# Optimization experiments

Measured on AMD Instinct MI355X. Metric: run time of the kernel, lower is better.

The kernel has to match this reference:

```python
import jax, jax.numpy as jnp
import numpy as np

B, T, D, H = 4096, 512, 5, 64
G = 4 * H  # i,f,g,o gates stacked (PyTorch order)
FC1, FC2 = 32, 1


def _uniform(key, shape, scale):
    return jax.random.uniform(key, shape, jnp.float32, -scale, scale)


def setup_inputs() -> dict:
    key = jax.random.key(0)
    ks = jax.random.split(key, 14)
    s = 1.0 / np.sqrt(H)  # torch LSTM/Linear init scale
    return {
        "x": jax.random.normal(ks[0], (B, T, D), jnp.float32),
        "W_ih0": _uniform(ks[1], (G, D), s),
        "W_hh0": _uniform(ks[2], (G, H), s),
        "b_ih0": _uniform(ks[3], (G,), s),
        "b_hh0": _uniform(ks[4], (G,), s),
        "W_ih1": _uniform(ks[5], (G, H), s),
        "W_hh1": _uniform(ks[6], (G, H), s),
        "b_ih1": _uniform(ks[7], (G,), s),
        "b_hh1": _uniform(ks[8], (G,), s),
        "W1": _uniform(ks[9], (FC1, H), s),
        "b1": _uniform(ks[10], (FC1,), s),
        "W2": _uniform(ks[11], (FC2, FC1), 1.0 / np.sqrt(FC1)),
        "b2": _uniform(ks[12], (FC2,), 1.0 / np.sqrt(FC1)),
    }


def lstm_layer(x, W_ih, W_hh, b_ih, b_hh):
    # x: [B,T,Din] -> (h_seq [B,T,H], h_T [B,H])
    b = x.shape[0]
    h = W_hh.shape[1]
    # precompute input contribution for all timesteps
    pre = jnp.einsum('btd,gd->btg', x, W_ih) + b_ih + b_hh  # [B,T,4H]

    def step(carry, xt):
        hs, cs = carry
        gates = xt + hs @ W_hh.T  # [B,4H]
        i, f, g, o = jnp.split(gates, 4, axis=-1)
        i = jax.nn.sigmoid(i)
        f = jax.nn.sigmoid(f)
        g = jnp.tanh(g)
        o = jax.nn.sigmoid(o)
        cs = f * cs + i * g
        hs = o * jnp.tanh(cs)
        return (hs, cs), hs

    h0 = jnp.zeros((b, h), x.dtype)
    (hT, cT), h_seq = jax.lax.scan(step, (h0, h0), jnp.swapaxes(pre, 0, 1))
    return jnp.swapaxes(h_seq, 0, 1), hT


def reference(x, W_ih0, W_hh0, b_ih0, b_hh0, W_ih1, W_hh1, b_ih1, b_hh1, W1, b1, W2, b2):
    # eval mode: dropout layers are identity
    h1_seq, _ = lstm_layer(x, W_ih0, W_hh0, b_ih0, b_hh0)
    _, h2_T = lstm_layer(h1_seq, W_ih1, W_hh1, b_ih1, b_hh1)  # h_n[-1]
    z = jax.nn.relu(h2_T @ W1.T + b1)  # [B,32]
    out = z @ W2.T + b2  # [B,1]
    return out.squeeze(-1)  # [B]
```

## Files before the change

### kernel.cpp

```cpp
#include <hip/hip_runtime.h>
#include <cstddef>

#define T_STEPS  512
#define D_IN     5
#define NB       16
#define NTHREADS 1024
#define LOG2E    1.4426950408889634f

typedef __attribute__((ext_vector_type(8))) short f16x8;
typedef __attribute__((ext_vector_type(4))) float f32x4;

#define MFMA_INIT(D, A, B, C) \
    asm("v_mfma_f32_16x16x32_f16 %0, %1, %2, %3" : "=&v"(D) : "a"(A), "v"(B), "v"(C))
#define MFMA_ACC(D, A, B) \
    asm("v_mfma_f32_16x16x32_f16 %0, %1, %2, %0" : "+v"(D) : "a"(A), "v"(B))

__device__ __forceinline__ short f2h(float f) {
    return (short)__builtin_bit_cast(unsigned short, (_Float16)f);
}

__device__ __forceinline__ float lstm_cell(const f32x4 acc, float& c) {
    const float tg = __builtin_amdgcn_exp2f(acc[2]);
    const float ui = __builtin_amdgcn_exp2f(-acc[0]);
    const float uf = __builtin_amdgcn_exp2f(-acc[1]);
    const float ig = (tg - 1.0f) * __builtin_amdgcn_rcpf((1.0f + ui) * (1.0f + tg));
    const float fz = __builtin_amdgcn_rcpf(1.0f + uf);
    c = fmaf(fz, c, ig);
    const float ca = fminf(c * (2.0f * LOG2E), 126.0f);
    const float tc = __builtin_amdgcn_exp2f(ca);
    const float uo = __builtin_amdgcn_exp2f(-acc[3]);
    return (tc - 1.0f) * __builtin_amdgcn_rcpf((1.0f + uo) * (1.0f + tc));
}

__device__ __forceinline__ int hswz(int n, int col) {
    return (((col >> 3) ^ (n & 7)) << 3) | (col & 7);
}

__global__ __launch_bounds__(NTHREADS, 4)
void lstm_stack_mfma7(const float* __restrict__ x,
                      const float* __restrict__ W_ih0,
                      const float* __restrict__ W_hh0,
                      const float* __restrict__ b_ih0,
                      const float* __restrict__ b_hh0,
                      const float* __restrict__ W_ih1,
                      const float* __restrict__ W_hh1,
                      const float* __restrict__ b_ih1,
                      const float* __restrict__ b_hh1,
                      const float* __restrict__ W1,
                      const float* __restrict__ b1,
                      const float* __restrict__ W2,
                      const float* __restrict__ b2,
                      float* __restrict__ out)
{
    __shared__ alignas(16) unsigned short h_hi[2][NB][128];
    __shared__ alignas(16) unsigned short x_pack[2][NB][40];
    __shared__ alignas(16) float h2f[NB][68];
    __shared__ alignas(16) float zb[NB][36];

    const int tid  = threadIdx.x;
    const int b0   = blockIdx.x * NB;
    const int w    = tid >> 6;
    const int lane = tid & 63;
    const int n16  = lane & 15;
    const int quad = lane >> 4;

    f16x8 aX;
    f16x8 a0[2];
    f16x8 a1[4];
    f32x4 bc0, bc1;
    float c0 = 0.f, c1 = 0.f;

    {
        const int u_a = w * 4 + (n16 >> 2);
        const int g_a = n16 & 3;
        const int r0  = g_a * 64 + u_a;
        const float sc = (g_a == 2) ? 2.0f * LOG2E : LOG2E;
        #pragma unroll
        for (int j = 0; j < 8; ++j) {
            const int k = quad * 8 + j;
            aX[j] = f2h(k < D_IN ? sc * W_ih0[r0 * D_IN + k] : 0.0f);
        }
        #pragma unroll
        for (int kt = 0; kt < 2; ++kt) {
            #pragma unroll
            for (int j = 0; j < 8; ++j)
                a0[kt][j] = f2h(sc * W_hh0[r0 * 64 + kt * 32 + quad * 8 + j]);
        }
        #pragma unroll
        for (int kt = 0; kt < 4; ++kt) {
            const int kg = kt * 32 + quad * 8;
            #pragma unroll
            for (int j = 0; j < 8; ++j)
                a1[kt][j] = f2h(sc * ((kg < 64) ? W_ih1[r0 * 64 + kg + j]
                                                : W_hh1[r0 * 64 + (kg - 64) + j]));
        }
        const int u_b = w * 4 + quad;
        #pragma unroll
        for (int r = 0; r < 4; ++r) {
            const float scr = (r == 2) ? 2.0f * LOG2E : LOG2E;
            bc0[r] = scr * (b_ih0[r * 64 + u_b] + b_hh0[r * 64 + u_b]);
            bc1[r] = scr * (b_ih1[r * 64 + u_b] + b_hh1[r * 64 + u_b]);
        }
    }

    for (int i = tid; i < 2 * NB * 128; i += NTHREADS) (&h_hi[0][0][0])[i] = 0;
    for (int i = tid; i < 2 * NB * 40; i += NTHREADS) (&x_pack[0][0][0])[i] = 0;
    __syncthreads();
    const int xb = tid / D_IN, xd = tid % D_IN;
    const bool xrole = (tid < NB * D_IN);
    if (xrole) {
        const float xv = x[((size_t)(b0 + xb) * T_STEPS) * D_IN + xd];
        x_pack[0][xb][xd] = (unsigned short)f2h(xv);
    }
    __syncthreads();

    const int u_c = w * 4 + quad;

    #pragma unroll 1
    for (int s = 0; s <= T_STEPS; ++s) {
        const int rb = s & 1, wbuf = rb ^ 1;

        float xv = 0.f;
        if (xrole && (s + 1) < T_STEPS)
            xv = x[((size_t)(b0 + xb) * T_STEPS + (s + 1)) * D_IN + xd];

        const f16x8 bxp = *reinterpret_cast<const f16x8*>(&x_pack[rb][n16][quad * 8]);
        f16x8 bhh[4];
        #pragma unroll
        for (int kt = 0; kt < 4; ++kt)
            bhh[kt] = *reinterpret_cast<const f16x8*>(
                &h_hi[rb][n16][((kt * 4 + quad) ^ (n16 & 7)) * 8]);

        f32x4 acc0, acc1;
        MFMA_INIT(acc0, aX, bxp, bc0);
        MFMA_ACC(acc0, a0[0], bhh[0]);
        MFMA_ACC(acc0, a0[1], bhh[1]);
        MFMA_INIT(acc1, a1[0], bhh[0], bc1);
        MFMA_ACC(acc1, a1[1], bhh[1]);
        MFMA_ACC(acc1, a1[2], bhh[2]);
        MFMA_ACC(acc1, a1[3], bhh[3]);

        asm("s_nop 7" : "+v"(acc0));
        if (s < T_STEPS) {
            const float h = lstm_cell(acc0, c0);
            h_hi[wbuf][n16][hswz(n16, u_c)] = (unsigned short)f2h(h);
        }

        asm("s_nop 7" : "+v"(acc1));
        if (s > 0) {
            const float h = lstm_cell(acc1, c1);
            h_hi[wbuf][n16][hswz(n16, 64 + u_c)] = (unsigned short)f2h(h);
            if (s == T_STEPS) h2f[n16][u_c] = h;
        }
        if (xrole && (s + 1) < T_STEPS)
            x_pack[wbuf][xb][xd] = (unsigned short)f2h(xv);
        __syncthreads();
    }

    if (tid < 512) {
        const int bb = tid >> 5;
        const int k  = tid & 31;
        float a = b1[k];
        #pragma unroll 16
        for (int j = 0; j < 64; ++j)
            a = fmaf(W1[k * 64 + j], h2f[bb][j], a);
        zb[bb][k] = fmaxf(a, 0.0f);
    }
    __syncthreads();
    if (tid < NB) {
        float a = b2[0];
        #pragma unroll
        for (int k = 0; k < 32; ++k) a = fmaf(W2[k], zb[tid][k], a);
        out[b0 + tid] = a;
    }
}

extern "C" void kernel_launch(void* const* d_in, const int* in_sizes, int n_in,
                              void* d_out, int out_size, void* d_ws, size_t ws_size,
                              hipStream_t stream) {
    (void)in_sizes; (void)n_in; (void)d_ws; (void)ws_size;
    const float* xp     = (const float*)d_in[0];
    const float* W_ih0  = (const float*)d_in[1];
    const float* W_hh0  = (const float*)d_in[2];
    const float* b_ih0  = (const float*)d_in[3];
    const float* b_hh0  = (const float*)d_in[4];
    const float* W_ih1  = (const float*)d_in[5];
    const float* W_hh1  = (const float*)d_in[6];
    const float* b_ih1  = (const float*)d_in[7];
    const float* b_hh1  = (const float*)d_in[8];
    const float* W1     = (const float*)d_in[9];
    const float* b1     = (const float*)d_in[10];
    const float* W2     = (const float*)d_in[11];
    const float* b2     = (const float*)d_in[12];
    float* outp = (float*)d_out;

    const int nblocks = out_size / NB;
    hipLaunchKernelGGL(lstm_stack_mfma7, dim3(nblocks), dim3(NTHREADS), 0, stream,
                       xp, W_ih0, W_hh0, b_ih0, b_hh0,
                       W_ih1, W_hh1, b_ih1, b_hh1,
                       W1, b1, W2, b2, outp);
}
```

Before: 533.4 us.

## Skew layer pipeline so off-critical-path MFMAs precompute next step's partial gates

```diff
diff --git a/kernel.cpp b/kernel.cpp
--- a/kernel.cpp
+++ b/kernel.cpp
@@ -23,21 +23,22 @@
     const float tg = __builtin_amdgcn_exp2f(acc[2]);
     const float ui = __builtin_amdgcn_exp2f(-acc[0]);
     const float uf = __builtin_amdgcn_exp2f(-acc[1]);
-    const float ig = (tg - 1.0f) * __builtin_amdgcn_rcpf((1.0f + ui) * (1.0f + tg));
-    const float fz = __builtin_amdgcn_rcpf(1.0f + uf);
-    c = fmaf(fz, c, ig);
+    const float A  = 1.0f + uf;
+    const float Bd = (1.0f + ui) * (1.0f + tg);
+    const float r  = __builtin_amdgcn_rcpf(A * Bd);
+    c = fmaf(c, Bd, (tg - 1.0f) * A) * r;
     const float ca = fminf(c * (2.0f * LOG2E), 126.0f);
     const float tc = __builtin_amdgcn_exp2f(ca);
     const float uo = __builtin_amdgcn_exp2f(-acc[3]);
     return (tc - 1.0f) * __builtin_amdgcn_rcpf((1.0f + uo) * (1.0f + tc));
 }
 
-__device__ __forceinline__ int hswz(int n, int col) {
-    return (((col >> 3) ^ (n & 7)) << 3) | (col & 7);
+__device__ __forceinline__ int hswz8(int n, int u) {
+    return (((u >> 3) ^ (n & 7)) << 3) | (u & 7);
 }
 
 __global__ __launch_bounds__(NTHREADS, 4)
-void lstm_stack_mfma7(const float* __restrict__ x,
+void lstm_stack_mfma8(const float* __restrict__ x,
                       const float* __restrict__ W_ih0,
                       const float* __restrict__ W_hh0,
                       const float* __restrict__ b_ih0,
@@ -52,7 +53,8 @@
                       const float* __restrict__ b2,
                       float* __restrict__ out)
 {
-    __shared__ alignas(16) unsigned short h_hi[2][NB][128];
+    __shared__ alignas(16) unsigned short h1b[2][NB][64];
+    __shared__ alignas(16) unsigned short h2b[2][NB][64];
     __shared__ alignas(16) unsigned short x_pack[2][NB][40];
     __shared__ alignas(16) float h2f[NB][68];
     __shared__ alignas(16) float zb[NB][36];
@@ -66,7 +68,8 @@
 
     f16x8 aX;
     f16x8 a0[2];
-    f16x8 a1[4];
+    f16x8 a1h1[2];
+    f16x8 a1h2[2];
     f32x4 bc0, bc1;
     float c0 = 0.f, c1 = 0.f;
 
@@ -83,16 +86,12 @@
         #pragma unroll
         for (int kt = 0; kt < 2; ++kt) {
             #pragma unroll
-            for (int j = 0; j < 8; ++j)
-                a0[kt][j] = f2h(sc * W_hh0[r0 * 64 + kt * 32 + quad * 8 + j]);
-        }
-        #pragma unroll
-        for (int kt = 0; kt < 4; ++kt) {
-            const int kg = kt * 32 + quad * 8;
-            #pragma unroll
-            for (int j = 0; j < 8; ++j)
-                a1[kt][j] = f2h(sc * ((kg < 64) ? W_ih1[r0 * 64 + kg + j]
-                                                : W_hh1[r0 * 64 + (kg - 64) + j]));
+            for (int j = 0; j < 8; ++j) {
+                const int kk = kt * 32 + quad * 8 + j;
+                a0[kt][j]   = f2h(sc * W_hh0[r0 * 64 + kk]);
+                a1h1[kt][j] = f2h(sc * W_ih1[r0 * 64 + kk]);
+                a1h2[kt][j] = f2h(sc * W_hh1[r0 * 64 + kk]);
+            }
         }
         const int u_b = w * 4 + quad;
         #pragma unroll
@@ -103,57 +102,70 @@
         }
     }
 
-    for (int i = tid; i < 2 * NB * 128; i += NTHREADS) (&h_hi[0][0][0])[i] = 0;
+    for (int i = tid; i < 2 * NB * 64; i += NTHREADS) (&h1b[0][0][0])[i] = 0;
+    for (int i = tid; i < 2 * NB * 64; i += NTHREADS) (&h2b[0][0][0])[i] = 0;
     for (int i = tid; i < 2 * NB * 40; i += NTHREADS) (&x_pack[0][0][0])[i] = 0;
     __syncthreads();
     const int xb = tid / D_IN, xd = tid % D_IN;
     const bool xrole = (tid < NB * D_IN);
     if (xrole) {
-        const float xv = x[((size_t)(b0 + xb) * T_STEPS) * D_IN + xd];
-        x_pack[0][xb][xd] = (unsigned short)f2h(xv);
+        const size_t base = (size_t)(b0 + xb) * T_STEPS;
+        x_pack[0][xb][xd] = (unsigned short)f2h(x[(base + 0) * D_IN + xd]);
+        x_pack[1][xb][xd] = (unsigned short)f2h(x[(base + 1) * D_IN + xd]);
     }
     __syncthreads();
 
     const int u_c = w * 4 + quad;
+    const int f0 = ((0 * 4 + quad) ^ (n16 & 7)) * 8;
+    const int f1 = ((1 * 4 + quad) ^ (n16 & 7)) * 8;
+    const int wo = hswz8(n16, u_c);
+
+    f32x4 pacc0, pacc1;
+    {
+        const f16x8 bx0 = *reinterpret_cast<const f16x8*>(&x_pack[0][n16][quad * 8]);
+        MFMA_INIT(pacc0, aX, bx0, bc0);
+        pacc1 = bc1;
+    }
 
     #pragma unroll 1
-    for (int s = 0; s <= T_STEPS; ++s) {
-        const int rb = s & 1, wbuf = rb ^ 1;
+    for (int t = 0; t <= T_STEPS + 1; ++t) {
+        const int p = t & 1, q = p ^ 1;
 
         float xv = 0.f;
-        if (xrole && (s + 1) < T_STEPS)
-            xv = x[((size_t)(b0 + xb) * T_STEPS + (s + 1)) * D_IN + xd];
-
-        const f16x8 bxp = *reinterpret_cast<const f16x8*>(&x_pack[rb][n16][quad * 8]);
-        f16x8 bhh[4];
-        #pragma unroll
-        for (int kt = 0; kt < 4; ++kt)
-            bhh[kt] = *reinterpret_cast<const f16x8*>(
-                &h_hi[rb][n16][((kt * 4 + quad) ^ (n16 & 7)) * 8]);
+        if (xrole && (t + 2) < T_STEPS)
+            xv = x[((size_t)(b0 + xb) * T_STEPS + (t + 2)) * D_IN + xd];
+
+        const unsigned short* h1r = &h1b[q][n16][0];
+        const unsigned short* h2r = &h2b[q][n16][0];
+        const f16x8 bx = *reinterpret_cast<const f16x8*>(&x_pack[q][n16][quad * 8]);
+        f16x8 bh1[2], bh2[2];
+        bh1[0] = *reinterpret_cast<const f16x8*>(h1r + f0);
+        bh1[1] = *reinterpret_cast<const f16x8*>(h1r + f1);
+        bh2[0] = *reinterpret_cast<const f16x8*>(h2r + f0);
+        bh2[1] = *reinterpret_cast<const f16x8*>(h2r + f1);
 
         f32x4 acc0, acc1;
-        MFMA_INIT(acc0, aX, bxp, bc0);
-        MFMA_ACC(acc0, a0[0], bhh[0]);
-        MFMA_ACC(acc0, a0[1], bhh[1]);
-        MFMA_INIT(acc1, a1[0], bhh[0], bc1);
-        MFMA_ACC(acc1, a1[1], bhh[1]);
-        MFMA_ACC(acc1, a1[2], bhh[2]);
-        MFMA_ACC(acc1, a1[3], bhh[3]);
-
-        asm("s_nop 7" : "+v"(acc0));
-        if (s < T_STEPS) {
+        MFMA_INIT(acc0, a0[0],   bh1[0], pacc0);
+        MFMA_ACC (acc0, a0[1],   bh1[1]);
+        MFMA_INIT(acc1, a1h2[0], bh2[0], pacc1);
+        MFMA_ACC (acc1, a1h2[1], bh2[1]);
+        MFMA_INIT(pacc0, aX,      bx,     bc0);
+        MFMA_INIT(pacc1, a1h1[0], bh1[0], bc1);
+        MFMA_ACC (pacc1, a1h1[1], bh1[1]);
+
+        asm("s_nop 7\n\ts_nop 7" : "+v"(acc0));
+        if (t < T_STEPS) {
             const float h = lstm_cell(acc0, c0);
-            h_hi[wbuf][n16][hswz(n16, u_c)] = (unsigned short)f2h(h);
-        }
-
-        asm("s_nop 7" : "+v"(acc1));
-        if (s > 0) {
+            h1b[p][n16][wo] = (unsigned short)f2h(h);
+        }
+        asm("s_nop 7\n\ts_nop 7" : "+v"(acc1));
+        if (t >= 2) {
             const float h = lstm_cell(acc1, c1);
-            h_hi[wbuf][n16][hswz(n16, 64 + u_c)] = (unsigned short)f2h(h);
-            if (s == T_STEPS) h2f[n16][u_c] = h;
-        }
-        if (xrole && (s + 1) < T_STEPS)
-            x_pack[wbuf][xb][xd] = (unsigned short)f2h(xv);
+            h2b[p][n16][wo] = (unsigned short)f2h(h);
+            if (t == T_STEPS + 1) h2f[n16][u_c] = h;
+        }
+        if (xrole && (t + 2) < T_STEPS)
+            x_pack[p][xb][xd] = (unsigned short)f2h(xv);
         __syncthreads();
     }
 
@@ -195,7 +207,7 @@
     float* outp = (float*)d_out;
 
     const int nblocks = out_size / NB;
-    hipLaunchKernelGGL(lstm_stack_mfma7, dim3(nblocks), dim3(NTHREADS), 0, stream,
+    hipLaunchKernelGGL(lstm_stack_mfma8, dim3(nblocks), dim3(NTHREADS), 0, stream,
                        xp, W_ih0, W_hh0, b_ih0, b_hh0,
                        W_ih1, W_hh1, b_ih1, b_hh1,
                        W1, b1, W2, b2, outp);
```

Result: faster. 516.0 us (-3.3%).
